# Performance work log

Measured on AMD Instinct MI355X. Metric: run time of the kernel, lower is better.

The kernel has to match this reference:

```python
import jax, jax.numpy as jnp
import numpy as np

N_RAYS = 8192
HIDDEN = 64
GEO = 15
DENSITY_SCALE = 1.0
MIN_NEAR = 0.05
AABB = np.array([-1.0, -1.0, -1.0, 1.0, 1.0, 1.0], dtype=np.float32)


def setup_inputs() -> dict:
    key = jax.random.key(0)
    ks = jax.random.split(key, 12)
    rays_o = (jax.random.uniform(ks[0], (1, N_RAYS, 3)) - 0.5) * 0.6  # origins inside aabb
    d = jax.random.normal(ks[1], (1, N_RAYS, 3))
    rays_d = d / jnp.linalg.norm(d, axis=-1, keepdims=True)
    return {
        "rays_o": rays_o.astype(jnp.float32),
        "rays_d": rays_d.astype(jnp.float32),
        "time": jax.random.uniform(ks[2], (1, 1), dtype=jnp.float32),
        "background_color": jax.random.uniform(ks[3], (3,), dtype=jnp.float32),
        "Wd1": jax.random.normal(ks[4], (4, HIDDEN), dtype=jnp.float32) * 0.5,
        "bd1": jnp.zeros((HIDDEN,), jnp.float32),
        "Wd2": jax.random.normal(ks[5], (HIDDEN, 1 + GEO), dtype=jnp.float32) * 0.1,
        "bd2": jnp.zeros((1 + GEO,), jnp.float32),
        "Wc1": jax.random.normal(ks[6], (3 + GEO, HIDDEN), dtype=jnp.float32) * 0.5,
        "bc1": jnp.zeros((HIDDEN,), jnp.float32),
        "Wc2": jax.random.normal(ks[7], (HIDDEN, 3), dtype=jnp.float32) * 0.5,
        "bc2": jnp.zeros((3,), jnp.float32),
        "num_steps": 64,
        "upsample_steps": 64,
    }


def near_far_from_aabb(rays_o, rays_d, aabb, min_near):
    inv_d = 1.0 / jnp.where(jnp.abs(rays_d) < 1e-9, 1e-9, rays_d)
    t0 = (aabb[:3] - rays_o) * inv_d
    t1 = (aabb[3:] - rays_o) * inv_d
    tmin = jnp.max(jnp.minimum(t0, t1), axis=-1)
    tmax = jnp.min(jnp.maximum(t0, t1), axis=-1)
    nears = jnp.maximum(tmin, min_near)
    fars = jnp.where(tmax < nears, nears + 1e-2, tmax)
    return nears, fars


def density_fn(x, t, Wd1, bd1, Wd2, bd2):
    # x: [M,3]; t: scalar time. sigma via exp (trunc_exp-style activation).
    inp = jnp.concatenate([x, jnp.ones_like(x[..., :1]) * t], axis=-1)
    h = jax.nn.relu(inp @ Wd1 + bd1) @ Wd2 + bd2
    return jnp.exp(h[..., 0]), h[..., 1:]


def color_fn(d, geo, Wc1, bc1, Wc2, bc2):
    h = jax.nn.relu(jnp.concatenate([d, geo], axis=-1) @ Wc1 + bc1)
    return jax.nn.sigmoid(h @ Wc2 + bc2)


def composite_weights(z_vals, sigma, sample_dist):
    deltas = z_vals[..., 1:] - z_vals[..., :-1]
    deltas = jnp.concatenate(
        [deltas, jnp.broadcast_to(sample_dist, deltas[..., :1].shape)], axis=-1)
    alphas = 1.0 - jnp.exp(-deltas * DENSITY_SCALE * sigma)
    shifted = jnp.concatenate(
        [jnp.ones_like(alphas[..., :1]), 1.0 - alphas + 1e-15], axis=-1)
    weights = alphas * jnp.cumprod(shifted, axis=-1)[..., :-1]
    return deltas, weights


def sample_pdf(bins, weights, n_samples):
    # bins: [N,T], weights: [N,T-1]; deterministic (det=True) inverse-CDF sampling.
    weights = weights + 1e-5
    pdf = weights / jnp.sum(weights, axis=-1, keepdims=True)
    cdf = jnp.cumsum(pdf, axis=-1)
    cdf = jnp.concatenate([jnp.zeros_like(cdf[..., :1]), cdf], axis=-1)  # [N,T]
    u = jnp.linspace(0.5 / n_samples, 1.0 - 0.5 / n_samples, n_samples, dtype=bins.dtype)
    u = jnp.broadcast_to(u, (bins.shape[0], n_samples))
    inds = jax.vmap(lambda c, uu: jnp.searchsorted(c, uu, side='right'))(cdf, u)
    below = jnp.clip(inds - 1, 0, cdf.shape[-1] - 1)
    above = jnp.clip(inds, 0, cdf.shape[-1] - 1)
    cdf_g0 = jnp.take_along_axis(cdf, below, axis=-1)
    cdf_g1 = jnp.take_along_axis(cdf, above, axis=-1)
    bins_g0 = jnp.take_along_axis(bins, jnp.clip(below, 0, bins.shape[-1] - 1), axis=-1)
    bins_g1 = jnp.take_along_axis(bins, jnp.clip(above, 0, bins.shape[-1] - 1), axis=-1)
    denom = cdf_g1 - cdf_g0
    denom = jnp.where(denom < 1e-5, 1.0, denom)
    t = (u - cdf_g0) / denom
    return bins_g0 + t * (bins_g1 - bins_g0)


def reference(rays_o, rays_d, time, background_color, Wd1, bd1, Wd2, bd2,
              Wc1, bc1, Wc2, bc2, num_steps, upsample_steps):
    prefix = rays_o.shape[:-1]
    rays_o = rays_o.reshape(-1, 3)
    rays_d = rays_d.reshape(-1, 3)
    N = rays_o.shape[0]
    aabb = jnp.asarray(AABB)
    t = time.reshape(())

    nears, fars = near_far_from_aabb(rays_o, rays_d, aabb, MIN_NEAR)
    nears = jax.lax.stop_gradient(nears)[:, None]
    fars = jax.lax.stop_gradient(fars)[:, None]

    z = jnp.linspace(0.0, 1.0, num_steps, dtype=rays_o.dtype)[None, :]
    z_vals = nears + (fars - nears) * z                      # [N,S]
    sample_dist = (fars - nears) / num_steps                 # [N,1]

    xyzs = rays_o[:, None, :] + rays_d[:, None, :] * z_vals[..., None]
    xyzs = jnp.clip(xyzs, aabb[:3], aabb[3:])
    sigma, geo = density_fn(xyzs.reshape(-1, 3), t, Wd1, bd1, Wd2, bd2)
    sigma = sigma.reshape(N, num_steps)
    geo = geo.reshape(N, num_steps, -1)

    # --- hierarchical importance sampling (no-grad branch in original) ---
    deltas, weights = composite_weights(
        jax.lax.stop_gradient(z_vals), jax.lax.stop_gradient(sigma), sample_dist)
    z_vals_mid = jax.lax.stop_gradient(z_vals)[..., :-1] + 0.5 * deltas[..., :-1]
    new_z_vals = jax.lax.stop_gradient(
        sample_pdf(z_vals_mid, weights[:, 1:-1], upsample_steps))
    new_xyzs = rays_o[:, None, :] + rays_d[:, None, :] * new_z_vals[..., None]
    new_xyzs = jax.lax.stop_gradient(jnp.clip(new_xyzs, aabb[:3], aabb[3:]))
    new_sigma, new_geo = density_fn(new_xyzs.reshape(-1, 3), t, Wd1, bd1, Wd2, bd2)
    new_sigma = new_sigma.reshape(N, upsample_steps)
    new_geo = new_geo.reshape(N, upsample_steps, -1)

    # --- merge coarse+fine by sorting along the ray ---
    z_all = jnp.concatenate([z_vals, new_z_vals], axis=1)
    order = jnp.argsort(z_all, axis=1)
    z_all = jnp.take_along_axis(z_all, order, axis=1)
    xyzs_all = jnp.take_along_axis(
        jnp.concatenate([xyzs, new_xyzs], axis=1), order[..., None], axis=1)
    sigma_all = jnp.take_along_axis(
        jnp.concatenate([sigma, new_sigma], axis=1), order, axis=1)
    geo_all = jnp.take_along_axis(
        jnp.concatenate([geo, new_geo], axis=1), order[..., None], axis=1)

    # --- alpha compositing ---
    _, weights = composite_weights(z_all, sigma_all, sample_dist)  # [N,S+U]
    dirs = jnp.broadcast_to(rays_d[:, None, :], xyzs_all.shape)
    mask = weights > 1e-4
    rgbs = color_fn(dirs.reshape(-1, 3), geo_all.reshape(-1, GEO),
                    Wc1, bc1, Wc2, bc2)
    rgbs = jnp.where(mask.reshape(-1, 1), rgbs, 0.0).reshape(N, -1, 3)

    weights_sum = jnp.sum(weights, axis=-1)
    image = jnp.sum(weights[..., None] * rgbs, axis=-2)
    image = image + (1.0 - weights_sum)[..., None] * background_color
    return image.reshape(*prefix, 3)
```

## Files before the change

kernel.cpp:

```cpp
#include <hip/hip_runtime.h>
#include <math.h>

#define NRAYS 8192

typedef __attribute__((ext_vector_type(8))) short bf16x8;
typedef __attribute__((ext_vector_type(4))) float f32x4;
typedef __attribute__((ext_vector_type(4))) unsigned u32x4;

#define FENCE asm volatile("" ::: "memory")

__device__ __forceinline__ short f2bf(float f) {
  union { float f; unsigned u; } v; v.f = f;
  unsigned r = (v.u + 0x7FFFu + ((v.u >> 16) & 1u)) >> 16;
  return (short)r;
}
__device__ __forceinline__ float bf2f(short s) {
  union { unsigned u; float f; } v; v.u = ((unsigned)(unsigned short)s) << 16;
  return v.f;
}
__device__ __forceinline__ unsigned cvt2(float a, float b) {
  unsigned r;
  asm("v_cvt_pk_bf16_f32 %0, %1, %2" : "=v"(r) : "v"(a), "v"(b));
  return r;
}
__device__ __forceinline__ unsigned cvtr(float a, float b) {
  return cvt2(fmaxf(a, 0.f), fmaxf(b, 0.f));
}
__device__ __forceinline__ float fast_rcp(float x) {
  float r;
  asm("v_rcp_f32 %0, %1" : "=v"(r) : "v"(x));
  return r;
}
__device__ __forceinline__ bf16x8 pack_b(unsigned a, unsigned b, unsigned c, unsigned d) {
  union { u32x4 u; bf16x8 v; } x;
  x.u = (u32x4){a, b, c, d};
  return x.v;
}
__device__ __forceinline__ float readlane63(float v) {
  return __int_as_float(__builtin_amdgcn_readlane(__float_as_int(v), 63));
}
__device__ __forceinline__ float zcoarse(float nearv, float span, int m) {
  return fmaf(span, (float)m * (1.f / 63.f), nearv);
}

#define UPD(OLD, SRC, CTRL, RMASK)                                        \
  __int_as_float(__builtin_amdgcn_update_dpp(                             \
      __float_as_int(OLD), __float_as_int(SRC), CTRL, RMASK, 0xf, false))

__device__ __forceinline__ float scan_mul_dpp(float v) {
  v *= UPD(1.f, v, 0x111, 0xf);
  v *= UPD(1.f, v, 0x112, 0xf);
  v *= UPD(1.f, v, 0x114, 0xf);
  v *= UPD(1.f, v, 0x118, 0xf);
  v *= UPD(1.f, v, 0x142, 0xa);
  v *= UPD(1.f, v, 0x143, 0xc);
  return v;
}
__device__ __forceinline__ float scan_add_dpp(float v) {
  v += UPD(0.f, v, 0x111, 0xf);
  v += UPD(0.f, v, 0x112, 0xf);
  v += UPD(0.f, v, 0x114, 0xf);
  v += UPD(0.f, v, 0x118, 0xf);
  v += UPD(0.f, v, 0x142, 0xa);
  v += UPD(0.f, v, 0x143, 0xc);
  return v;
}
__device__ __forceinline__ float red_add_dpp(float v) {
  v += UPD(0.f, v, 0xB1, 0xf);
  v += UPD(0.f, v, 0x4E, 0xf);
  v += UPD(0.f, v, 0x141, 0xf);
  v += UPD(0.f, v, 0x140, 0xf);
  v += UPD(0.f, v, 0x142, 0xa);
  v += UPD(0.f, v, 0x143, 0xc);
  return v;
}

__global__ void pack_weights(const float* __restrict__ Wd1, const float* __restrict__ bd1,
                             const float* __restrict__ Wd2, const float* __restrict__ Wc1,
                             const float* __restrict__ bc1, const float* __restrict__ Wc2,
                             short* __restrict__ pk) {
  const int l = threadIdx.x;
  const int g = l >> 4, c = l & 15;
  for (int m = 0; m < 4; ++m) {
    int nu = 16 * m + c;
    short e[8] = {0, 0, 0, 0, 0, 0, 0, 0};
    if (g == 0) {
      for (int i = 0; i < 4; ++i) {
        short h = f2bf(Wd1[i * 64 + nu]);
        e[i] = h;
        e[4 + i] = h;
      }
    } else if (g == 1) {
      for (int i = 0; i < 4; ++i) {
        float w = Wd1[i * 64 + nu];
        e[i] = f2bf(w - bf2f(f2bf(w)));
      }
      e[4] = f2bf(bd1[nu]);
    }
    for (int i = 0; i < 8; ++i) pk[m * 512 + l * 8 + i] = e[i];
  }
  for (int kt = 0; kt < 2; ++kt)
    for (int i = 0; i < 8; ++i) {
      int nu = 32 * kt + 16 * (i >> 2) + 4 * g + (i & 3);
      pk[2048 + kt * 512 + l * 8 + i] = f2bf(Wd2[nu * 16 + c]);
    }
  for (int m = 0; m < 4; ++m) {
    int nu = 16 * m + c;
    for (int i = 0; i < 8; ++i) {
      int k = 8 * g + i;
      short e = 0;
      if (k >= 1 && k <= 15) e = f2bf(Wc1[(2 + k) * 64 + nu]);
      else if (k >= 16 && k <= 18) e = f2bf(Wc1[(k - 16) * 64 + nu]);
      else if (k == 19) e = f2bf(bc1[nu]);
      pk[3072 + m * 512 + l * 8 + i] = e;
    }
  }
  for (int kt = 0; kt < 2; ++kt)
    for (int i = 0; i < 8; ++i) {
      int nu = 32 * kt + 16 * (i >> 2) + 4 * g + (i & 3);
      pk[5120 + kt * 512 + l * 8 + i] = (c < 3) ? f2bf(Wc2[nu * 3 + c]) : (short)0;
    }
}

__device__ __forceinline__ float density_pass(
    const short* __restrict__ pk, short* __restrict__ Xd, short* __restrict__ Xc,
    int lane, int g, int c, float x, float y, float z, float tf, float tLoF,
    const float* __restrict__ bd2g, int xcBase) {
  {
    unsigned w0 = cvt2(x, y);
    unsigned w1 = cvt2(z, tf);
    union { unsigned u; float f; } ux, uy, uz;
    ux.u = w0 << 16; uy.u = w0 & 0xFFFF0000u; uz.u = w1 << 16;
    unsigned w2 = cvt2(x - ux.f, y - uy.f);
    unsigned w3 = cvt2(z - uz.f, tLoF);
    u32x4 pv; pv[0] = w0; pv[1] = w1; pv[2] = w2; pv[3] = w3;
    *(u32x4*)&Xd[lane * 8] = pv;
  }
  FENCE;

  bf16x8 A1[4];
#pragma unroll
  for (int m = 0; m < 4; ++m) A1[m] = *(const bf16x8*)(pk + m * 512 + lane * 8);

  unsigned P[2][4][4];
#pragma unroll
  for (int mh = 0; mh < 2; ++mh) {
    f32x4 a0[4], a1[4];
#pragma unroll
    for (int n = 0; n < 4; ++n) {
      a0[n] = (f32x4){0.f, 0.f, 0.f, 0.f};
      a1[n] = (f32x4){0.f, 0.f, 0.f, 0.f};
    }
#pragma unroll
    for (int n = 0; n < 4; ++n) {
      bf16x8 v = *(const bf16x8*)&Xd[(16 * n + c) * 8];
      if (g == 1) v[4] = (short)0x3F80;
      a0[n] = __builtin_amdgcn_mfma_f32_16x16x32_bf16(A1[2 * mh], v, a0[n], 0, 0, 0);
      a1[n] = __builtin_amdgcn_mfma_f32_16x16x32_bf16(A1[2 * mh + 1], v, a1[n], 0, 0, 0);
    }
#pragma unroll
    for (int n = 0; n < 4; ++n) {
      P[mh][n][0] = cvtr(a0[n][0], a0[n][1]);
      P[mh][n][1] = cvtr(a0[n][2], a0[n][3]);
      P[mh][n][2] = cvtr(a1[n][0], a1[n][1]);
      P[mh][n][3] = cvtr(a1[n][2], a1[n][3]);
    }
  }

  bf16x8 A2[2];
  A2[0] = *(const bf16x8*)(pk + 2048 + lane * 8);
  A2[1] = *(const bf16x8*)(pk + 2048 + 512 + lane * 8);
  f32x4 o[4];
#pragma unroll
  for (int n = 0; n < 4; ++n) o[n] = (f32x4){0.f, 0.f, 0.f, 0.f};
#pragma unroll
  for (int n = 0; n < 4; ++n)
#pragma unroll
    for (int kt = 0; kt < 2; ++kt)
      o[n] = __builtin_amdgcn_mfma_f32_16x16x32_bf16(
          A2[kt], pack_b(P[kt][n][0], P[kt][n][1], P[kt][n][2], P[kt][n][3]), o[n], 0, 0, 0);

  const float4 bd2v = *(const float4*)&bd2g[4 * g];
#pragma unroll
  for (int n = 0; n < 4; ++n) {
    o[n][0] += bd2v.x; o[n][1] += bd2v.y; o[n][2] += bd2v.z; o[n][3] += bd2v.w;
  }
#pragma unroll
  for (int n = 0; n < 4; ++n) {
    short* xr = Xc + (xcBase + 16 * n + c) * 16 + 4 * g;
    *(unsigned*)(xr + 0) = cvt2(o[n][0], o[n][1]);
    *(unsigned*)(xr + 2) = cvt2(o[n][2], o[n][3]);
  }
  FENCE;
  float t0 = __shfl(o[0][0], c);
  float t1 = __shfl(o[1][0], c);
  float t2 = __shfl(o[2][0], c);
  float t3 = __shfl(o[3][0], c);
  return (g == 0) ? t0 : (g == 1) ? t1 : (g == 2) ? t2 : t3;
}

__global__ __launch_bounds__(64, 4) void nerf_render(
    const float* __restrict__ rays_o, const float* __restrict__ rays_d,
    const float* __restrict__ time_p, const float* __restrict__ bg,
    const float* __restrict__ bd2g, const float* __restrict__ bc2g,
    const short* __restrict__ pk, float* __restrict__ out) {
  __shared__ __align__(64) char smem[7168];
  short* Xc  = (short*)smem;
  short* Xd  = (short*)(smem + 4096);
  float* zsl = (float*)(smem + 5120);
  float* ssl = (float*)(smem + 5632);
  float* cdfl = (float*)(smem + 6144);
  float* nzl  = (float*)(smem + 6400);
  float* wul  = (float*)(smem + 6144);
  float* wsl  = (float*)(smem + 6656);

  const int lane = threadIdx.x;
  const int g = lane >> 4, c = lane & 15;
  const int ray = blockIdx.x;

  const float tf = time_p[0];
  union { unsigned u; float f; } th; th.u = cvt2(tf, tf) << 16;
  const float tLoF = tf - th.f;
  const float o0 = rays_o[ray * 3 + 0], o1 = rays_o[ray * 3 + 1], o2 = rays_o[ray * 3 + 2];
  const float d0 = rays_d[ray * 3 + 0], d1 = rays_d[ray * 3 + 1], d2 = rays_d[ray * 3 + 2];

  float nearv, farv;
  {
    float i0 = fast_rcp((fabsf(d0) < 1e-9f) ? 1e-9f : d0);
    float i1 = fast_rcp((fabsf(d1) < 1e-9f) ? 1e-9f : d1);
    float i2 = fast_rcp((fabsf(d2) < 1e-9f) ? 1e-9f : d2);
    float a0 = (-1.f - o0) * i0, b0 = (1.f - o0) * i0;
    float a1 = (-1.f - o1) * i1, b1 = (1.f - o1) * i1;
    float a2 = (-1.f - o2) * i2, b2 = (1.f - o2) * i2;
    float tmin = fmaxf(fmaxf(fminf(a0, b0), fminf(a1, b1)), fminf(a2, b2));
    float tmax = fminf(fminf(fmaxf(a0, b0), fmaxf(a1, b1)), fmaxf(a2, b2));
    nearv = fmaxf(tmin, 0.05f);
    farv = (tmax < nearv) ? (nearv + 1e-2f) : tmax;
  }
  const float span = farv - nearv;
  const float sd = span * (1.f / 64.f);

  const float zi = zcoarse(nearv, span, lane);
  float cx = fminf(fmaxf(fmaf(d0, zi, o0), -1.f), 1.f);
  float cy = fminf(fmaxf(fmaf(d1, zi, o1), -1.f), 1.f);
  float cz = fminf(fmaxf(fmaf(d2, zi, o2), -1.f), 1.f);
  float sraw = density_pass(pk, Xd, Xc, lane, g, c, cx, cy, cz, tf, tLoF, bd2g, 0);
  const float sigma = __expf(sraw);

  const float znext = __shfl_down(zi, 1, 64);
  const float cdelta = (lane < 63) ? (znext - zi) : sd;
  const float calpha = 1.f - __expf(-cdelta * sigma);
  {
    float T = 1.f - calpha + 1e-15f;
    float Pincl = scan_mul_dpp(T);
    float Pexcl = __shfl_up(Pincl, 1, 64);
    if (lane == 0) Pexcl = 1.f;
    float wgt = calpha * Pexcl;
    float v = (lane >= 1 && lane <= 62) ? (wgt + 1e-5f) : 0.f;
    float S = scan_add_dpp(v);
    float inv_tot = fast_rcp(readlane63(S));
    if (lane < 63) cdfl[lane] = S * inv_tot;
  }
  FENCE;

  float nzv;
  {
    const float u = ((float)lane + 0.5f) * 0.015625f;
    int lo = 0, hi = 63;
    while (lo < hi) {
      int m = (lo + hi) >> 1;
      if (cdfl[m] <= u) lo = m + 1; else hi = m;
    }
    int below = lo - 1;
    int above = (lo < 62) ? lo : 62;
    float c0 = cdfl[below], c1 = cdfl[above];
    float b0 = 0.5f * (zcoarse(nearv, span, below) + zcoarse(nearv, span, below + 1));
    float b1 = 0.5f * (zcoarse(nearv, span, above) + zcoarse(nearv, span, above + 1));
    float dn = c1 - c0;
    dn = (dn < 1e-5f) ? 1.f : dn;
    nzv = fmaf((u - c0) * fast_rcp(dn), (b1 - b0), b0);
  }
  nzl[lane] = nzv;
  FENCE;

  float fx = fminf(fmaxf(fmaf(d0, nzv, o0), -1.f), 1.f);
  float fy = fminf(fmaxf(fmaf(d1, nzv, o1), -1.f), 1.f);
  float fz = fminf(fmaxf(fmaf(d2, nzv, o2), -1.f), 1.f);
  float nsraw = density_pass(pk, Xd, Xc, lane, g, c, fx, fy, fz, tf, tLoF, bd2g, 64);
  const float nsigma = __expf(nsraw);
  FENCE;

  int r1, r2;
  {
    int lo = 0, hi = 64;
    while (lo < hi) { int m = (lo + hi) >> 1; if (nzl[m] < zi) lo = m + 1; else hi = m; }
    r1 = lane + lo;
  }
  {
    int lo = 0, hi = 64;
    while (lo < hi) {
      int m = (lo + hi) >> 1;
      if (zcoarse(nearv, span, m) <= nzv) lo = m + 1; else hi = m;
    }
    r2 = lane + lo;
  }
  FENCE;
  zsl[r1] = zi;  ssl[r1] = sigma;
  zsl[r2] = nzv; ssl[r2] = nsigma;
  FENCE;

  float w0, w1, wsum;
  {
    float z0 = zsl[lane];
    float z0n = zsl[lane + 1];
    float z1 = zsl[lane + 64];
    float dl0 = z0n - z0;
    float dl1 = (lane < 63) ? (zsl[lane + 65] - z1) : sd;
    float al0 = 1.f - __expf(-dl0 * ssl[lane]);
    float al1 = 1.f - __expf(-dl1 * ssl[lane + 64]);
    float T0 = 1.f - al0 + 1e-15f;
    float T1 = 1.f - al1 + 1e-15f;
    float P0 = scan_mul_dpp(T0);
    float P1 = scan_mul_dpp(T1);
    float prodLo = readlane63(P0);
    float e0 = __shfl_up(P0, 1, 64);
    float e1 = __shfl_up(P1, 1, 64);
    if (lane == 0) { e0 = 1.f; e1 = 1.f; }
    w0 = al0 * e0;
    w1 = al1 * prodLo * e1;
    wsum = red_add_dpp(w0 + w1);
    wsl[lane] = w0;
    wsl[lane + 64] = w1;
  }
  FENCE;

  const float wc = wsl[r1];
  const float wf = wsl[r2];
  FENCE;
  wul[lane] = wc;
  wul[64 + lane] = wf;
  const unsigned long long mC = __ballot(wc > 1e-4f);
  const unsigned long long mF = __ballot(wf > 1e-4f);
  FENCE;

  bf16x8 CA[4];
#pragma unroll
  for (int m = 0; m < 4; ++m) CA[m] = *(const bf16x8*)(pk + 3072 + m * 512 + lane * 8);
  bf16x8 C2A[2];
  C2A[0] = *(const bf16x8*)(pk + 5120 + lane * 8);
  C2A[1] = *(const bf16x8*)(pk + 5120 + 512 + lane * 8);
  const float bc20 = bc2g[0], bc21 = bc2g[1], bc22 = bc2g[2];
  const bf16x8 bD = pack_b(cvt2(d0, d1), cvt2(d2, 1.0f), 0u, 0u);
  const bf16x8 bZ = pack_b(0u, 0u, 0u, 0u);
  const int xoffs = (g < 2) ? 8 * g : 0;

  float cr = 0.f, cgr = 0.f, cb = 0.f;
#pragma unroll
  for (int half = 0; half < 2; ++half) {
    const unsigned long long mm = half ? mF : mC;
#pragma unroll
    for (int n = 0; n < 4; ++n) {
      if ((mm >> (16 * n)) & 0xFFFFull) {
        bf16x8 ld = *(const bf16x8*)&Xc[(64 * half + 16 * n + c) * 16 + xoffs];
        bf16x8 V = (g < 2) ? ld : ((g == 2) ? bD : bZ);
        f32x4 a[4];
#pragma unroll
        for (int m = 0; m < 4; ++m) {
          a[m] = (f32x4){0.f, 0.f, 0.f, 0.f};
          a[m] = __builtin_amdgcn_mfma_f32_16x16x32_bf16(CA[m], V, a[m], 0, 0, 0);
        }
        f32x4 oc = (f32x4){0.f, 0.f, 0.f, 0.f};
#pragma unroll
        for (int kt = 0; kt < 2; ++kt) {
          bf16x8 Bh = pack_b(cvtr(a[2 * kt][0], a[2 * kt][1]),
                             cvtr(a[2 * kt][2], a[2 * kt][3]),
                             cvtr(a[2 * kt + 1][0], a[2 * kt + 1][1]),
                             cvtr(a[2 * kt + 1][2], a[2 * kt + 1][3]));
          oc = __builtin_amdgcn_mfma_f32_16x16x32_bf16(C2A[kt], Bh, oc, 0, 0, 0);
        }
        if (g == 0) {
          float wgt = wul[64 * half + 16 * n + c];
          if (wgt > 1e-4f) {
            cr  += wgt * fast_rcp(1.f + __expf(-(oc[0] + bc20)));
            cgr += wgt * fast_rcp(1.f + __expf(-(oc[1] + bc21)));
            cb  += wgt * fast_rcp(1.f + __expf(-(oc[2] + bc22)));
          }
        }
      }
    }
  }

  cr = red_add_dpp(cr);
  cgr = red_add_dpp(cgr);
  cb = red_add_dpp(cb);

  if (lane == 63) {
    const float rem = 1.f - wsum;
    out[ray * 3 + 0] = cr + rem * bg[0];
    out[ray * 3 + 1] = cgr + rem * bg[1];
    out[ray * 3 + 2] = cb + rem * bg[2];
  }
}

extern "C" void kernel_launch(void* const* d_in, const int* in_sizes, int n_in,
                              void* d_out, int out_size, void* d_ws, size_t ws_size,
                              hipStream_t stream) {
  const float* rays_o = (const float*)d_in[0];
  const float* rays_d = (const float*)d_in[1];
  const float* time_p = (const float*)d_in[2];
  const float* bg     = (const float*)d_in[3];
  const float* Wd1    = (const float*)d_in[4];
  const float* bd1    = (const float*)d_in[5];
  const float* Wd2    = (const float*)d_in[6];
  const float* bd2    = (const float*)d_in[7];
  const float* Wc1    = (const float*)d_in[8];
  const float* bc1    = (const float*)d_in[9];
  const float* Wc2    = (const float*)d_in[10];
  const float* bc2    = (const float*)d_in[11];

  short* pk = (short*)d_ws;
  pack_weights<<<1, 64, 0, stream>>>(Wd1, bd1, Wd2, Wc1, bc1, Wc2, pk);
  nerf_render<<<NRAYS, 64, 0, stream>>>(rays_o, rays_d, time_p, bg, bd2, bc2, pk,
                                        (float*)d_out);
}
```

Baseline: 39.08 us.

## Replace LDS scratch arrays with wave shuffles and shrink shared memory

Keeps the CDF, fine z values and per-sample weights in registers and reads them through cross-lane shuffles instead of LDS stores and loads. The binary searches become fixed-trip unrolled loops built on shuffles. This cuts the LDS footprint from 7168 to 5120 bytes, and the launch-bounds occupancy hint rises from 4 to 7 blocks. In exchange there are more shuffle instructions (each bpermute still goes through LDS hardware) and possibly more register pressure under the tighter occupancy target.

```diff
diff --git a/kernel.cpp b/kernel.cpp
--- a/kernel.cpp
+++ b/kernel.cpp
@@ -199,20 +199,16 @@
   return (g == 0) ? t0 : (g == 1) ? t1 : (g == 2) ? t2 : t3;
 }
 
-__global__ __launch_bounds__(64, 4) void nerf_render(
+__global__ __launch_bounds__(64, 7) void nerf_render(
     const float* __restrict__ rays_o, const float* __restrict__ rays_d,
     const float* __restrict__ time_p, const float* __restrict__ bg,
     const float* __restrict__ bd2g, const float* __restrict__ bc2g,
     const short* __restrict__ pk, float* __restrict__ out) {
-  __shared__ __align__(64) char smem[7168];
+  __shared__ __align__(64) char smem[5120];
   short* Xc  = (short*)smem;
   short* Xd  = (short*)(smem + 4096);
-  float* zsl = (float*)(smem + 5120);
-  float* ssl = (float*)(smem + 5632);
-  float* cdfl = (float*)(smem + 6144);
-  float* nzl  = (float*)(smem + 6400);
-  float* wul  = (float*)(smem + 6144);
-  float* wsl  = (float*)(smem + 6656);
+  float* zsl = (float*)(smem + 4096);
+  float* ssl = (float*)(smem + 4608);
 
   const int lane = threadIdx.x;
   const int g = lane >> 4, c = lane & 15;
@@ -247,10 +243,11 @@
   float sraw = density_pass(pk, Xd, Xc, lane, g, c, cx, cy, cz, tf, tLoF, bd2g, 0);
   const float sigma = __expf(sraw);
 
-  const float znext = __shfl_down(zi, 1, 64);
-  const float cdelta = (lane < 63) ? (znext - zi) : sd;
-  const float calpha = 1.f - __expf(-cdelta * sigma);
-  {
+  float cdfS;
+  {
+    const float znext = __shfl_down(zi, 1, 64);
+    const float cdelta = (lane < 63) ? (znext - zi) : sd;
+    const float calpha = 1.f - __expf(-cdelta * sigma);
     float T = 1.f - calpha + 1e-15f;
     float Pincl = scan_mul_dpp(T);
     float Pexcl = __shfl_up(Pincl, 1, 64);
@@ -258,30 +255,29 @@
     float wgt = calpha * Pexcl;
     float v = (lane >= 1 && lane <= 62) ? (wgt + 1e-5f) : 0.f;
     float S = scan_add_dpp(v);
-    float inv_tot = fast_rcp(readlane63(S));
-    if (lane < 63) cdfl[lane] = S * inv_tot;
-  }
-  FENCE;
+    cdfS = S * fast_rcp(readlane63(S));
+  }
 
   float nzv;
   {
     const float u = ((float)lane + 0.5f) * 0.015625f;
     int lo = 0, hi = 63;
-    while (lo < hi) {
-      int m = (lo + hi) >> 1;
-      if (cdfl[m] <= u) lo = m + 1; else hi = m;
+#pragma unroll
+    for (int it = 0; it < 6; ++it) {
+      int mid = (lo + hi) >> 1;
+      float v = __shfl(cdfS, mid, 64);
+      if (lo < hi) { if (v <= u) lo = mid + 1; else hi = mid; }
     }
     int below = lo - 1;
     int above = (lo < 62) ? lo : 62;
-    float c0 = cdfl[below], c1 = cdfl[above];
+    float c0 = __shfl(cdfS, below, 64);
+    float c1 = __shfl(cdfS, above, 64);
     float b0 = 0.5f * (zcoarse(nearv, span, below) + zcoarse(nearv, span, below + 1));
     float b1 = 0.5f * (zcoarse(nearv, span, above) + zcoarse(nearv, span, above + 1));
     float dn = c1 - c0;
     dn = (dn < 1e-5f) ? 1.f : dn;
     nzv = fmaf((u - c0) * fast_rcp(dn), (b1 - b0), b0);
   }
-  nzl[lane] = nzv;
-  FENCE;
 
   float fx = fminf(fmaxf(fmaf(d0, nzv, o0), -1.f), 1.f);
   float fy = fminf(fmaxf(fmaf(d1, nzv, o1), -1.f), 1.f);
@@ -293,14 +289,20 @@
   int r1, r2;
   {
     int lo = 0, hi = 64;
-    while (lo < hi) { int m = (lo + hi) >> 1; if (nzl[m] < zi) lo = m + 1; else hi = m; }
+#pragma unroll
+    for (int it = 0; it < 7; ++it) {
+      int mid = (lo + hi) >> 1;
+      float v = __shfl(nzv, mid, 64);
+      if (lo < hi) { if (v < zi) lo = mid + 1; else hi = mid; }
+    }
     r1 = lane + lo;
   }
   {
     int lo = 0, hi = 64;
-    while (lo < hi) {
-      int m = (lo + hi) >> 1;
-      if (zcoarse(nearv, span, m) <= nzv) lo = m + 1; else hi = m;
+#pragma unroll
+    for (int it = 0; it < 7; ++it) {
+      int mid = (lo + hi) >> 1;
+      if (lo < hi) { if (zcoarse(nearv, span, mid) <= nzv) lo = mid + 1; else hi = mid; }
     }
     r2 = lane + lo;
   }
@@ -329,19 +331,16 @@
     w0 = al0 * e0;
     w1 = al1 * prodLo * e1;
     wsum = red_add_dpp(w0 + w1);
-    wsl[lane] = w0;
-    wsl[lane + 64] = w1;
-  }
-  FENCE;
-
-  const float wc = wsl[r1];
-  const float wf = wsl[r2];
-  FENCE;
-  wul[lane] = wc;
-  wul[64 + lane] = wf;
+  }
+
+  float wlo = __shfl(w0, r1 & 63, 64);
+  float whi = __shfl(w1, r1 & 63, 64);
+  const float wc = (r1 < 64) ? wlo : whi;
+  wlo = __shfl(w0, r2 & 63, 64);
+  whi = __shfl(w1, r2 & 63, 64);
+  const float wf = (r2 < 64) ? wlo : whi;
   const unsigned long long mC = __ballot(wc > 1e-4f);
   const unsigned long long mF = __ballot(wf > 1e-4f);
-  FENCE;
 
   bf16x8 CA[4];
 #pragma unroll
@@ -358,9 +357,11 @@
 #pragma unroll
   for (int half = 0; half < 2; ++half) {
     const unsigned long long mm = half ? mF : mC;
+    const float wcf = half ? wf : wc;
 #pragma unroll
     for (int n = 0; n < 4; ++n) {
       if ((mm >> (16 * n)) & 0xFFFFull) {
+        float wgt = __shfl(wcf, 16 * n + c, 64);
         bf16x8 ld = *(const bf16x8*)&Xc[(64 * half + 16 * n + c) * 16 + xoffs];
         bf16x8 V = (g < 2) ? ld : ((g == 2) ? bD : bZ);
         f32x4 a[4];
@@ -378,13 +379,10 @@
                              cvtr(a[2 * kt + 1][2], a[2 * kt + 1][3]));
           oc = __builtin_amdgcn_mfma_f32_16x16x32_bf16(C2A[kt], Bh, oc, 0, 0, 0);
         }
-        if (g == 0) {
-          float wgt = wul[64 * half + 16 * n + c];
-          if (wgt > 1e-4f) {
-            cr  += wgt * fast_rcp(1.f + __expf(-(oc[0] + bc20)));
-            cgr += wgt * fast_rcp(1.f + __expf(-(oc[1] + bc21)));
-            cb  += wgt * fast_rcp(1.f + __expf(-(oc[2] + bc22)));
-          }
+        if (g == 0 && wgt > 1e-4f) {
+          cr  += wgt * fast_rcp(1.f + __expf(-(oc[0] + bc20)));
+          cgr += wgt * fast_rcp(1.f + __expf(-(oc[1] + bc21)));
+          cb  += wgt * fast_rcp(1.f + __expf(-(oc[2] + bc22)));
         }
       }
     }
```

Result: slower. 53.01 us (+35.7%).
